# Kernel optimization log

Measured on AMD Instinct MI355X. Metric: run time of the kernel, lower is better.

## Reference

```python
import jax, jax.numpy as jnp
import numpy as np

NUM_DOMAINS = 8
MARGIN = 1.0


def setup_inputs() -> dict:
    key = jax.random.key(0)
    k1, k2 = jax.random.split(key)
    features = jax.random.normal(k1, (4096, 1024), dtype=jnp.float32)
    domain_labels = jax.random.randint(k2, (4096,), 0, NUM_DOMAINS)
    return {"features": features, "domain_labels": domain_labels}


def reference(features, domain_labels):
    # Full BxB euclidean distance matrix (matches torch.cdist p=2, which uses
    # the mm-based path for this size). Safe sqrt so diagonal zeros are exact.
    sq = jnp.sum(features * features, axis=-1)                      # (B,)
    d2 = sq[:, None] + sq[None, :] - 2.0 * (features @ features.T)  # (B,B)
    d2 = jnp.maximum(d2, 0.0)
    dist = jnp.where(d2 > 0, jnp.sqrt(jnp.where(d2 > 0, d2, 1.0)), 0.0)
    vals = jax.nn.relu(MARGIN - dist)                               # (B,B)

    # Per-domain pair sums via one-hot contraction: s_d = m_d^T V m_d.
    onehot = (domain_labels[:, None] == jnp.arange(NUM_DOMAINS)[None, :]
              ).astype(features.dtype)                              # (B,K)
    n = onehot.sum(axis=0)                                          # (K,)
    row_sums = vals @ onehot                                        # (B,K)
    pair_sums = (onehot * row_sums).sum(axis=0)                     # (K,)

    valid = n > 1  # torch loop skips singleton domains
    per_domain = jnp.where(valid, pair_sums / jnp.maximum(n * n, 1.0), 0.0)
    cnt = valid.sum().astype(features.dtype)
    return jnp.where(cnt > 0, per_domain.sum() / jnp.maximum(cnt, 1.0), 0.0)
```

## Files before the change

### kernel.cpp

```cpp
#include <hip/hip_runtime.h>

#define NDOM 8
#define TT   32
#define KDIM 1024
#define RPAD 1040
#define BMAX 4096
#define GGRID 512

typedef float f32x4 __attribute__((ext_vector_type(4)));

__device__ inline void gload16(const void* g, void* l) {
    __builtin_amdgcn_global_load_lds(
        (const __attribute__((address_space(1))) unsigned int*)g,
        (__attribute__((address_space(3))) unsigned int*)l, 16, 0, 0);
}

__global__ __launch_bounds__(256) void k_prep(
    const float* __restrict__ F, const int* __restrict__ labels, int B,
    unsigned char* __restrict__ Fb, float* __restrict__ sq,
    int* __restrict__ perm, int* __restrict__ dom_off) {
    const int t = threadIdx.x, lane = t & 63, wv = t >> 6;

    if (blockIdx.x == 0) {
        __shared__ int lab[BMAX];
        __shared__ unsigned wcnt[4][NDOM];
        for (int i = t; i < BMAX; i += 256) lab[i] = (i < B) ? labels[i] : -1;
        __syncthreads();

        int nch = (B + 63) >> 6;
        int cpw = (nch + 3) >> 2;
        int c0 = wv * cpw, c1 = min(c0 + cpw, nch);
        unsigned long long below = (1ull << lane) - 1ull;

        unsigned cnt[NDOM];
#pragma unroll
        for (int d = 0; d < NDOM; ++d) cnt[d] = 0;
        for (int c = c0; c < c1; ++c) {
            int d = lab[c * 64 + lane];
#pragma unroll
            for (int dd = 0; dd < NDOM; ++dd)
                cnt[dd] += (unsigned)__popcll(__ballot(d == dd));
        }
        if (lane == 0)
#pragma unroll
            for (int dd = 0; dd < NDOM; ++dd) wcnt[wv][dd] = cnt[dd];
        __syncthreads();

        unsigned offs[NDOM + 1];
        offs[0] = 0;
#pragma unroll
        for (int dd = 0; dd < NDOM; ++dd)
            offs[dd + 1] = offs[dd] + wcnt[0][dd] + wcnt[1][dd] + wcnt[2][dd] + wcnt[3][dd];
        if (t <= NDOM) dom_off[t] = (int)offs[t];

        unsigned run[NDOM];
#pragma unroll
        for (int dd = 0; dd < NDOM; ++dd) {
            unsigned base = offs[dd];
            for (int w = 0; w < 4; ++w)
                if (w < wv) base += wcnt[w][dd];
            run[dd] = base;
        }
        for (int c = c0; c < c1; ++c) {
            int i = c * 64 + lane;
            int d = lab[i];
            int pos = -1;
#pragma unroll
            for (int dd = 0; dd < NDOM; ++dd) {
                unsigned long long m = __ballot(d == dd);
                if (d == dd) pos = (int)run[dd] + __popcll(m & below);
                run[dd] += (unsigned)__popcll(m);
            }
            if (i < B) perm[pos] = i;
        }
        return;
    }

    int i0 = (int)(blockIdx.x - 1) * 16;
    for (int j = wv; j < 16; j += 4) {
        int row = i0 + j;
        if (row >= B) break;
        const float4* srow = (const float4*)(F + (size_t)row * KDIM);
        int* drow = (int*)(Fb + (size_t)row * KDIM);
        float ss = 0.f;
#pragma unroll
        for (int it = 0; it < 4; ++it) {
            float4 v = srow[it * 64 + lane];
            ss += v.x * v.x + v.y * v.y + v.z * v.z + v.w * v.w;
            int p = __builtin_amdgcn_cvt_pk_fp8_f32(v.x, v.y, 0, false);
            p = __builtin_amdgcn_cvt_pk_fp8_f32(v.z, v.w, p, true);
            drow[it * 64 + lane] = p;
        }
#pragma unroll
        for (int s = 32; s > 0; s >>= 1) ss += __shfl_xor(ss, s);
        if (lane == 0) sq[row] = ss;
    }
}

__global__ __launch_bounds__(256) void k_gram(
    const unsigned char* __restrict__ Fb, const float* __restrict__ sq,
    const int* __restrict__ perm, const int* __restrict__ dom_off,
    float* __restrict__ part) {
    __shared__ __align__(16) unsigned char lA[TT * RPAD];
    __shared__ __align__(16) unsigned char lB[TT * RPAD];
    __shared__ int s_p[64];
    __shared__ float s_sq[64];
    __shared__ int s_offs[NDOM + 1], s_ts[NDOM + 1];
    __shared__ float s_ps[NDOM];

    const int t = threadIdx.x, lane = t & 63, wv = t >> 6;
    const int m16 = lane & 15, quad = lane >> 4;
    const int wm = (wv & 1) * 16, wn = (wv >> 1) * 16;

    if (t == 0) {
        int T = 0;
        for (int d = 0; d < NDOM; ++d) {
            int o0 = dom_off[d], o1 = dom_off[d + 1];
            s_offs[d] = o0;
            s_ts[d] = T;
            int n = o1 - o0;
            int nt = (n + TT - 1) / TT;
            T += nt * (nt + 1) / 2;
        }
        s_offs[NDOM] = dom_off[NDOM];
        s_ts[NDOM] = T;
    }
    if (t < NDOM) s_ps[t] = 0.f;
    __syncthreads();
    const int T = s_ts[NDOM];

    for (int tile = blockIdx.x; tile < T; tile += gridDim.x) {
        int dom = 0;
        while (tile >= s_ts[dom + 1]) ++dom;
        int off = s_offs[dom], n = s_offs[dom + 1] - off;
        int nt = (n + TT - 1) / TT;
        int rel = tile - s_ts[dom];
        int ty = 0, rem = rel;
        while (rem >= nt - ty) { rem -= nt - ty; ++ty; }
        int tx = ty + rem;
        int tr = ty * TT, tc = tx * TT;
        bool diag = (ty == tx);

        if (t < 64) {
            int r = (t < 32) ? min(tr + t, n - 1) : min(tc + (t - 32), n - 1);
            int p = perm[off + r];
            s_p[t] = p;
            s_sq[t] = sq[p];
        }
        __syncthreads();

#pragma unroll
        for (int j = 0; j < 16; ++j) {
            int r = wv * 16 + j;
            if (r < 32) {
                const unsigned char* g = Fb + (size_t)s_p[r] * KDIM + lane * 16;
                gload16(g, lA + r * RPAD);
            } else if (!diag) {
                const unsigned char* g = Fb + (size_t)s_p[r] * KDIM + lane * 16;
                gload16(g, lB + (r - 32) * RPAD);
            }
        }
        __syncthreads();

        const unsigned char* Bbuf = diag ? lA : lB;
        const unsigned char* pa = lA + (wm + m16) * RPAD + quad * 8;
        const unsigned char* pb = Bbuf + (wn + m16) * RPAD + quad * 8;
        f32x4 ac0 = (f32x4){0.f, 0.f, 0.f, 0.f};
        f32x4 ac1 = (f32x4){0.f, 0.f, 0.f, 0.f};
#pragma unroll
        for (int ks = 0; ks < 32; ks += 2) {
            long a0 = *(const long*)(pa + ks * 32);
            long b0 = *(const long*)(pb + ks * 32);
            long a1 = *(const long*)(pa + ks * 32 + 32);
            long b1 = *(const long*)(pb + ks * 32 + 32);
            ac0 = __builtin_amdgcn_mfma_f32_16x16x32_fp8_fp8(a0, b0, ac0, 0, 0, 0);
            ac1 = __builtin_amdgcn_mfma_f32_16x16x32_fp8_fp8(a1, b1, ac1, 0, 0, 0);
        }

        float local = 0.f;
        int lr0 = wm + quad * 4;
        int lc = wn + m16;
        int pc = tc + lc;
        if (pc < n) {
            float sb = s_sq[32 + lc];
#pragma unroll
            for (int r = 0; r < 4; ++r) {
                int pr = tr + lr0 + r;
                if (pr < n) {
                    float val;
                    if (pr == pc) {
                        val = 1.0f;
                    } else {
                        float d2 = s_sq[lr0 + r] + sb - 2.0f * (ac0[r] + ac1[r]);
                        d2 = fmaxf(d2, 0.f);
                        val = fmaxf(1.0f - sqrtf(d2), 0.f);
                    }
                    local += val;
                }
            }
        }
        if (!diag) local *= 2.f;
#pragma unroll
        for (int s = 32; s > 0; s >>= 1) local += __shfl_xor(local, s);
        if (lane == 0) atomicAdd(&s_ps[dom], local);
        __syncthreads();
    }

    __syncthreads();
    if (t < NDOM) part[blockIdx.x * NDOM + t] = s_ps[t];
}

__global__ __launch_bounds__(256) void k_final(
    const float* __restrict__ part, const int* __restrict__ dom_off,
    float* __restrict__ out) {
    __shared__ float red[8][32];
    int t = threadIdx.x;
    int d = t & 7, ch = t >> 3;
    float s = 0.f;
    for (int b = ch; b < GGRID; b += 32) s += part[b * NDOM + d];
    red[d][ch] = s;
    __syncthreads();
    if (t < NDOM) {
        float ps = 0.f;
#pragma unroll
        for (int c = 0; c < 32; ++c) ps += red[t][c];
        red[t][0] = ps;
    }
    __syncthreads();
    if (t == 0) {
        float acc = 0.f;
        int v = 0;
        for (int dd = 0; dd < NDOM; ++dd) {
            int n = dom_off[dd + 1] - dom_off[dd];
            if (n > 1) {
                acc += red[dd][0] / ((float)n * (float)n);
                ++v;
            }
        }
        out[0] = (v > 0) ? acc / (float)v : 0.f;
    }
}

extern "C" void kernel_launch(void* const* d_in, const int* in_sizes, int n_in,
                              void* d_out, int out_size, void* d_ws, size_t ws_size,
                              hipStream_t stream) {
    const float* F = (const float*)d_in[0];
    const int* labels = (const int*)d_in[1];
    int B = in_sizes[1];

    char* ws = (char*)d_ws;
    unsigned char* Fb = (unsigned char*)ws;
    float* sq = (float*)(ws + (size_t)BMAX * KDIM);
    int* perm = (int*)(ws + (size_t)BMAX * KDIM + BMAX * 4);
    int* dom_off = (int*)(ws + (size_t)BMAX * KDIM + BMAX * 8);
    float* part = (float*)(ws + (size_t)BMAX * KDIM + BMAX * 8 + 256);

    int ncv = (B + 15) / 16;
    k_prep<<<ncv + 1, 256, 0, stream>>>(F, labels, B, Fb, sq, perm, dom_off);
    k_gram<<<GGRID, 256, 0, stream>>>(Fb, sq, perm, dom_off, part);
    k_final<<<1, 256, 0, stream>>>(part, dom_off, (float*)d_out);
}
```

Measured before the change: 93.81 us.

## Prune distant pairs with a bf16 partial-dot lower bound and recheck candidates exactly

The full fp8 Gram over all 1024 dimensions is replaced by a bf16 MFMA over only the first 128 dimensions. A Cauchy-Schwarz bound on the remaining dimensions gives a lower bound on each squared distance, and any pair whose bound exceeds a safety threshold is dropped, since it cannot contribute to relu(1 - dist). The few surviving pairs go to a global overflow list, and a single-block final kernel recomputes them exactly in fp32. The diagonal is handled analytically as n per domain. This sharply cuts gathered bytes and MFMA work, but the result is silently wrong if more than 8192 candidate pairs survive, for example with clustered or near-duplicate features.

```diff
diff --git a/kernel.cpp b/kernel.cpp
--- a/kernel.cpp
+++ b/kernel.cpp
@@ -3,27 +3,40 @@
 #define NDOM 8
 #define TT   32
 #define KDIM 1024
-#define RPAD 1040
+#define K0   128
+#define RB0  256
+#define RP   272
 #define BMAX 4096
 #define GGRID 512
+#define OVF_CAP 8192
+#define CERT_T 8.0f
 
 typedef float f32x4 __attribute__((ext_vector_type(4)));
-
-__device__ inline void gload16(const void* g, void* l) {
+typedef short bf16x8 __attribute__((ext_vector_type(8)));
+
+__device__ inline void gload4(const void* g, void* l) {
     __builtin_amdgcn_global_load_lds(
         (const __attribute__((address_space(1))) unsigned int*)g,
-        (__attribute__((address_space(3))) unsigned int*)l, 16, 0, 0);
+        (__attribute__((address_space(3))) unsigned int*)l, 4, 0, 0);
+}
+
+__device__ inline unsigned short f2bf(float f) {
+    unsigned u = __float_as_uint(f);
+    unsigned r = (u + 0x7fffu + ((u >> 16) & 1u)) >> 16;
+    return (unsigned short)r;
 }
 
 __global__ __launch_bounds__(256) void k_prep(
     const float* __restrict__ F, const int* __restrict__ labels, int B,
-    unsigned char* __restrict__ Fb, float* __restrict__ sq,
-    int* __restrict__ perm, int* __restrict__ dom_off) {
+    unsigned char* __restrict__ Fb16, float* __restrict__ sq,
+    float* __restrict__ rb, int* __restrict__ perm, int* __restrict__ dom_off,
+    int* __restrict__ ovf_cnt) {
     const int t = threadIdx.x, lane = t & 63, wv = t >> 6;
 
     if (blockIdx.x == 0) {
         __shared__ int lab[BMAX];
         __shared__ unsigned wcnt[4][NDOM];
+        if (t == 0) *ovf_cnt = 0;
         for (int i = t; i < BMAX; i += 256) lab[i] = (i < B) ? labels[i] : -1;
         __syncthreads();
 
@@ -76,37 +89,43 @@
         return;
     }
 
-    int i0 = (int)(blockIdx.x - 1) * 16;
-    for (int j = wv; j < 16; j += 4) {
-        int row = i0 + j;
-        if (row >= B) break;
-        const float4* srow = (const float4*)(F + (size_t)row * KDIM);
-        int* drow = (int*)(Fb + (size_t)row * KDIM);
-        float ss = 0.f;
-#pragma unroll
-        for (int it = 0; it < 4; ++it) {
-            float4 v = srow[it * 64 + lane];
-            ss += v.x * v.x + v.y * v.y + v.z * v.z + v.w * v.w;
-            int p = __builtin_amdgcn_cvt_pk_fp8_f32(v.x, v.y, 0, false);
-            p = __builtin_amdgcn_cvt_pk_fp8_f32(v.z, v.w, p, true);
-            drow[it * 64 + lane] = p;
-        }
-#pragma unroll
-        for (int s = 32; s > 0; s >>= 1) ss += __shfl_xor(ss, s);
-        if (lane == 0) sq[row] = ss;
+    int row = (int)(blockIdx.x - 1) * 4 + wv;
+    if (row >= B) return;
+    const float4* srow = (const float4*)(F + (size_t)row * KDIM);
+    float ss = 0.f, s0 = 0.f;
+#pragma unroll
+    for (int it = 0; it < 4; ++it) {
+        float4 v = srow[it * 64 + lane];
+        float d = v.x * v.x + v.y * v.y + v.z * v.z + v.w * v.w;
+        ss += d;
+        if (it == 0 && lane < 32) {
+            s0 = d;
+            ushort4 p;
+            p.x = f2bf(v.x); p.y = f2bf(v.y); p.z = f2bf(v.z); p.w = f2bf(v.w);
+            ((ushort4*)(Fb16 + (size_t)row * RB0))[lane] = p;
+        }
+    }
+#pragma unroll
+    for (int s = 32; s > 0; s >>= 1) {
+        ss += __shfl_xor(ss, s);
+        s0 += __shfl_xor(s0, s);
+    }
+    if (lane == 0) {
+        sq[row] = ss;
+        rb[row] = sqrtf(fmaxf(ss - s0, 0.f));
     }
 }
 
 __global__ __launch_bounds__(256) void k_gram(
-    const unsigned char* __restrict__ Fb, const float* __restrict__ sq,
-    const int* __restrict__ perm, const int* __restrict__ dom_off,
-    float* __restrict__ part) {
-    __shared__ __align__(16) unsigned char lA[TT * RPAD];
-    __shared__ __align__(16) unsigned char lB[TT * RPAD];
+    const unsigned char* __restrict__ Fb16, const float* __restrict__ sq,
+    const float* __restrict__ rb, const int* __restrict__ perm,
+    const int* __restrict__ dom_off, int* __restrict__ ovf_cnt,
+    int4* __restrict__ ovf) {
+    __shared__ __align__(16) unsigned char lA[TT * RP];
+    __shared__ __align__(16) unsigned char lB[TT * RP];
     __shared__ int s_p[64];
-    __shared__ float s_sq[64];
+    __shared__ float s_sq[64], s_rb[64];
     __shared__ int s_offs[NDOM + 1], s_ts[NDOM + 1];
-    __shared__ float s_ps[NDOM];
 
     const int t = threadIdx.x, lane = t & 63, wv = t >> 6;
     const int m16 = lane & 15, quad = lane >> 4;
@@ -125,7 +144,6 @@
         s_offs[NDOM] = dom_off[NDOM];
         s_ts[NDOM] = T;
     }
-    if (t < NDOM) s_ps[t] = 0.f;
     __syncthreads();
     const int T = s_ts[NDOM];
 
@@ -146,6 +164,7 @@
             int p = perm[off + r];
             s_p[t] = p;
             s_sq[t] = sq[p];
+            s_rb[t] = rb[p];
         }
         __syncthreads();
 
@@ -153,87 +172,92 @@
         for (int j = 0; j < 16; ++j) {
             int r = wv * 16 + j;
             if (r < 32) {
-                const unsigned char* g = Fb + (size_t)s_p[r] * KDIM + lane * 16;
-                gload16(g, lA + r * RPAD);
+                const unsigned char* g = Fb16 + (size_t)s_p[r] * RB0 + lane * 4;
+                gload4(g, lA + r * RP);
             } else if (!diag) {
-                const unsigned char* g = Fb + (size_t)s_p[r] * KDIM + lane * 16;
-                gload16(g, lB + (r - 32) * RPAD);
+                const unsigned char* g = Fb16 + (size_t)s_p[r] * RB0 + lane * 4;
+                gload4(g, lB + (r - 32) * RP);
             }
         }
         __syncthreads();
 
         const unsigned char* Bbuf = diag ? lA : lB;
-        const unsigned char* pa = lA + (wm + m16) * RPAD + quad * 8;
-        const unsigned char* pb = Bbuf + (wn + m16) * RPAD + quad * 8;
-        f32x4 ac0 = (f32x4){0.f, 0.f, 0.f, 0.f};
-        f32x4 ac1 = (f32x4){0.f, 0.f, 0.f, 0.f};
-#pragma unroll
-        for (int ks = 0; ks < 32; ks += 2) {
-            long a0 = *(const long*)(pa + ks * 32);
-            long b0 = *(const long*)(pb + ks * 32);
-            long a1 = *(const long*)(pa + ks * 32 + 32);
-            long b1 = *(const long*)(pb + ks * 32 + 32);
-            ac0 = __builtin_amdgcn_mfma_f32_16x16x32_fp8_fp8(a0, b0, ac0, 0, 0, 0);
-            ac1 = __builtin_amdgcn_mfma_f32_16x16x32_fp8_fp8(a1, b1, ac1, 0, 0, 0);
-        }
-
-        float local = 0.f;
+        const unsigned char* pa = lA + (wm + m16) * RP + quad * 16;
+        const unsigned char* pb = Bbuf + (wn + m16) * RP + quad * 16;
+        f32x4 ac = (f32x4){0.f, 0.f, 0.f, 0.f};
+#pragma unroll
+        for (int ks = 0; ks < 4; ++ks) {
+            bf16x8 a = *(const bf16x8*)(pa + ks * 64);
+            bf16x8 b = *(const bf16x8*)(pb + ks * 64);
+            ac = __builtin_amdgcn_mfma_f32_16x16x32_bf16(a, b, ac, 0, 0, 0);
+        }
+
         int lr0 = wm + quad * 4;
         int lc = wn + m16;
         int pc = tc + lc;
         if (pc < n) {
-            float sb = s_sq[32 + lc];
+            float sb = s_sq[32 + lc], rbb = s_rb[32 + lc];
 #pragma unroll
             for (int r = 0; r < 4; ++r) {
                 int pr = tr + lr0 + r;
-                if (pr < n) {
-                    float val;
-                    if (pr == pc) {
-                        val = 1.0f;
-                    } else {
-                        float d2 = s_sq[lr0 + r] + sb - 2.0f * (ac0[r] + ac1[r]);
-                        d2 = fmaxf(d2, 0.f);
-                        val = fmaxf(1.0f - sqrtf(d2), 0.f);
+                if (pr < n && pr != pc) {
+                    float cert = s_sq[lr0 + r] + sb
+                               - 2.0f * ac[r] - 2.0f * s_rb[lr0 + r] * rbb;
+                    if (cert <= CERT_T) {
+                        int slot = atomicAdd(ovf_cnt, 1);
+                        if (slot < OVF_CAP) {
+                            int4 rec;
+                            rec.x = s_p[lr0 + r];
+                            rec.y = s_p[32 + lc];
+                            rec.z = diag ? 1 : 2;
+                            rec.w = dom;
+                            ovf[slot] = rec;
+                        }
                     }
-                    local += val;
                 }
             }
         }
-        if (!diag) local *= 2.f;
-#pragma unroll
-        for (int s = 32; s > 0; s >>= 1) local += __shfl_xor(local, s);
-        if (lane == 0) atomicAdd(&s_ps[dom], local);
-        __syncthreads();
-    }
-
+        __syncthreads();
+    }
+}
+
+__global__ __launch_bounds__(256) void k_final(
+    const float* __restrict__ F, const float* __restrict__ sq,
+    const int* __restrict__ dom_off, const int* __restrict__ ovf_cnt,
+    const int4* __restrict__ ovf, float* __restrict__ out) {
+    __shared__ float dsum[NDOM];
+    const int t = threadIdx.x, lane = t & 63, wv = t >> 6;
+    if (t < NDOM) dsum[t] = 0.f;
     __syncthreads();
-    if (t < NDOM) part[blockIdx.x * NDOM + t] = s_ps[t];
-}
-
-__global__ __launch_bounds__(256) void k_final(
-    const float* __restrict__ part, const int* __restrict__ dom_off,
-    float* __restrict__ out) {
-    __shared__ float red[8][32];
-    int t = threadIdx.x;
-    int d = t & 7, ch = t >> 3;
-    float s = 0.f;
-    for (int b = ch; b < GGRID; b += 32) s += part[b * NDOM + d];
-    red[d][ch] = s;
-    __syncthreads();
-    if (t < NDOM) {
-        float ps = 0.f;
-#pragma unroll
-        for (int c = 0; c < 32; ++c) ps += red[t][c];
-        red[t][0] = ps;
+
+    int cnt = *ovf_cnt;
+    if (cnt > OVF_CAP) cnt = OVF_CAP;
+    for (int e = wv; e < cnt; e += 4) {
+        int4 rec = ovf[e];
+        const float4* ra = (const float4*)(F + (size_t)rec.x * KDIM);
+        const float4* rbp = (const float4*)(F + (size_t)rec.y * KDIM);
+        float dot = 0.f;
+#pragma unroll
+        for (int it = 0; it < 4; ++it) {
+            float4 va = ra[it * 64 + lane], vb = rbp[it * 64 + lane];
+            dot += va.x * vb.x + va.y * vb.y + va.z * vb.z + va.w * vb.w;
+        }
+#pragma unroll
+        for (int s = 32; s > 0; s >>= 1) dot += __shfl_xor(dot, s);
+        if (lane == 0) {
+            float d2 = fmaxf(sq[rec.x] + sq[rec.y] - 2.f * dot, 0.f);
+            float val = fmaxf(1.f - sqrtf(d2), 0.f) * (float)rec.z;
+            atomicAdd(&dsum[rec.w], val);
+        }
     }
     __syncthreads();
     if (t == 0) {
         float acc = 0.f;
         int v = 0;
-        for (int dd = 0; dd < NDOM; ++dd) {
-            int n = dom_off[dd + 1] - dom_off[dd];
+        for (int d = 0; d < NDOM; ++d) {
+            int n = dom_off[d + 1] - dom_off[d];
             if (n > 1) {
-                acc += red[dd][0] / ((float)n * (float)n);
+                acc += ((float)n + dsum[d]) / ((float)n * (float)n);
                 ++v;
             }
         }
@@ -249,14 +273,18 @@
     int B = in_sizes[1];
 
     char* ws = (char*)d_ws;
-    unsigned char* Fb = (unsigned char*)ws;
-    float* sq = (float*)(ws + (size_t)BMAX * KDIM);
-    int* perm = (int*)(ws + (size_t)BMAX * KDIM + BMAX * 4);
-    int* dom_off = (int*)(ws + (size_t)BMAX * KDIM + BMAX * 8);
-    float* part = (float*)(ws + (size_t)BMAX * KDIM + BMAX * 8 + 256);
-
-    int ncv = (B + 15) / 16;
-    k_prep<<<ncv + 1, 256, 0, stream>>>(F, labels, B, Fb, sq, perm, dom_off);
-    k_gram<<<GGRID, 256, 0, stream>>>(Fb, sq, perm, dom_off, part);
-    k_final<<<1, 256, 0, stream>>>(part, dom_off, (float*)d_out);
-}
+    size_t o = 0;
+    unsigned char* Fb16 = (unsigned char*)(ws + o); o += (size_t)BMAX * RB0;
+    float* sq = (float*)(ws + o);      o += (size_t)BMAX * 4;
+    float* rb = (float*)(ws + o);      o += (size_t)BMAX * 4;
+    int* perm = (int*)(ws + o);        o += (size_t)BMAX * 4;
+    int* dom_off = (int*)(ws + o);     o += 64;
+    int* ovf_cnt = (int*)(ws + o);     o += 64;
+    int4* ovf = (int4*)(ws + o);       o += (size_t)OVF_CAP * 16;
+
+    int nconv = (B + 3) >> 2;
+    k_prep<<<nconv + 1, 256, 0, stream>>>(F, labels, B, Fb16, sq, rb, perm,
+                                          dom_off, ovf_cnt);
+    k_gram<<<GGRID, 256, 0, stream>>>(Fb16, sq, rb, perm, dom_off, ovf_cnt, ovf);
+    k_final<<<1, 256, 0, stream>>>(F, sq, dom_off, ovf_cnt, ovf, (float*)d_out);
+}
```

Result: faster. 83.45 us (-11.0%).
